# Kernel optimization log

Measured on AMD Instinct MI355X. Metric: run time of the kernel, lower is better.

## Reference

```python
import jax, jax.numpy as jnp
import numpy as np

N = 100000        # nodes
E = 1600000       # edges
G = 128           # graphs in batch
D_FEAT = 240      # continuous node features (input_features - 1)
EMB = 16          # node-type embedding dim
H = 256           # hidden size (both layers)
PH = 128          # pool / classifier hidden
GF = 32           # global feature dim
LN_EPS = 1e-5


def setup_inputs() -> dict:
    key = jax.random.key(0)
    ks = jax.random.split(key, 24)

    node_types = jax.random.randint(ks[0], (N,), 0, 400).astype(jnp.float32)
    feats = jax.random.normal(ks[1], (N, D_FEAT), dtype=jnp.float32)
    x = jnp.concatenate([node_types[:, None], feats], axis=1)  # [N, 241]

    edge_index = jax.random.randint(ks[2], (2, E), 0, N, dtype=jnp.int32)
    batch = jnp.sort(jax.random.randint(ks[3], (N,), 0, G, dtype=jnp.int32))
    global_features = jax.random.normal(ks[4], (G, GF), dtype=jnp.float32)

    s = 0.05
    p = {}
    p['emb_table'] = jax.random.normal(ks[5], (400, EMB), dtype=jnp.float32) * s
    # layer 0 GIN MLP (in=256 -> 256 -> 256) + LayerNorm
    p['l0_w1'] = jax.random.normal(ks[6], (H, H), dtype=jnp.float32) * s
    p['l0_b1'] = jnp.zeros((H,), jnp.float32)
    p['l0_w2'] = jax.random.normal(ks[7], (H, H), dtype=jnp.float32) * s
    p['l0_b2'] = jnp.zeros((H,), jnp.float32)
    p['ln0_g'] = jnp.ones((H,), jnp.float32)
    p['ln0_b'] = jnp.zeros((H,), jnp.float32)
    # layer 1
    p['l1_w1'] = jax.random.normal(ks[8], (H, H), dtype=jnp.float32) * s
    p['l1_b1'] = jnp.zeros((H,), jnp.float32)
    p['l1_w2'] = jax.random.normal(ks[9], (H, H), dtype=jnp.float32) * s
    p['l1_b2'] = jnp.zeros((H,), jnp.float32)
    p['ln1_g'] = jnp.ones((H,), jnp.float32)
    p['ln1_b'] = jnp.zeros((H,), jnp.float32)
    # attentional aggregation gate: 256 -> 128 -> 1
    p['gate_w1'] = jax.random.normal(ks[10], (H, PH), dtype=jnp.float32) * s
    p['gate_b1'] = jnp.zeros((PH,), jnp.float32)
    p['gate_w2'] = jax.random.normal(ks[11], (PH, 1), dtype=jnp.float32) * s
    p['gate_b2'] = jnp.zeros((1,), jnp.float32)
    # classifier: 256+32 -> 128 -> 2
    p['cls_w1'] = jax.random.normal(ks[12], (H + GF, PH), dtype=jnp.float32) * s
    p['cls_b1'] = jnp.zeros((PH,), jnp.float32)
    p['cls_w2'] = jax.random.normal(ks[13], (PH, 2), dtype=jnp.float32) * s
    p['cls_b2'] = jnp.zeros((2,), jnp.float32)

    return dict(x=x, edge_index=edge_index, batch=batch,
                global_features=global_features, **p)


def _layernorm(z, g, b):
    mu = jnp.mean(z, axis=-1, keepdims=True)
    var = jnp.mean(jnp.square(z - mu), axis=-1, keepdims=True)
    return (z - mu) * jax.lax.rsqrt(var + LN_EPS) * g + b


def _gin_block(h, src, dst, w1, b1, w2, b2, ln_g, ln_b):
    # GINConv, eps=0: mlp((1+eps)*x_i + sum_{j->i} x_j)
    agg = jax.ops.segment_sum(h[src], dst, num_segments=h.shape[0])
    z = h + agg
    z = jax.nn.relu(z @ w1 + b1) @ w2 + b2
    z = jax.nn.relu(_layernorm(z, ln_g, ln_b))
    return h + z  # dropout is identity in eval; residual


def reference(x, edge_index, batch, global_features, emb_table,
              l0_w1, l0_b1, l0_w2, l0_b2, ln0_g, ln0_b,
              l1_w1, l1_b1, l1_w2, l1_b2, ln1_g, ln1_b,
              gate_w1, gate_b1, gate_w2, gate_b2,
              cls_w1, cls_b1, cls_w2, cls_b2):
    node_types = x[:, 0].astype(jnp.int32)
    h = jnp.concatenate([x[:, 1:], emb_table[node_types]], axis=1)  # [N, 256]

    src, dst = edge_index[0], edge_index[1]
    h = _gin_block(h, src, dst, l0_w1, l0_b1, l0_w2, l0_b2, ln0_g, ln0_b)
    h = _gin_block(h, src, dst, l1_w1, l1_b1, l1_w2, l1_b2, ln1_g, ln1_b)

    # AttentionalAggregation: segment softmax over gate scores, weighted sum
    gate = jax.nn.relu(h @ gate_w1 + gate_b1) @ gate_w2 + gate_b2  # [N, 1]
    gate = gate[:, 0]
    m = jax.ops.segment_max(gate, batch, num_segments=G)
    a = jnp.exp(gate - m[batch])
    s = jax.ops.segment_sum(a, batch, num_segments=G)
    w = a / s[batch]
    pooled = jax.ops.segment_sum(w[:, None] * h, batch, num_segments=G)  # [G, 256]

    z = jnp.concatenate([pooled, global_features], axis=1)  # [G, 288]
    out = jax.nn.relu(z @ cls_w1 + cls_b1) @ cls_w2 + cls_b2  # [G, 2]
    return out
```

## Files before the change

kernel.cpp:

```cpp
#include <hip/hip_runtime.h>
#include <math.h>

#define N_NODES 100000
#define N_EDGES 1600000
#define NG      128
#define HD      256
#define PHD     128
#define GFD     32
#define XW      241
#define LN_EPS  1e-5f
#define SLOT    64

typedef __attribute__((ext_vector_type(8))) short bf8_t;
typedef __attribute__((ext_vector_type(4))) float f4_t;

static __device__ __forceinline__ float relu_f(float x){ return fmaxf(x, 0.0f); }

static __device__ __forceinline__ unsigned short f2bf_rn(float v) {
    unsigned int u = __float_as_uint(v);
    unsigned int r = (u + 0x7fffu + ((u >> 16) & 1u)) >> 16;
    return (unsigned short)r;
}
static __device__ __forceinline__ float bf2f(unsigned short h) {
    return __uint_as_float((unsigned int)h << 16);
}

__global__ void build_h_kernel(const float* __restrict__ x, const float* __restrict__ emb,
                               float* __restrict__ h, unsigned short* __restrict__ h16)
{
    int node = blockIdx.x;
    int tid  = threadIdx.x;
    const float* xr = x + (size_t)node * XW;
    float v;
    if (tid < 240) {
        v = xr[1 + tid];
    } else {
        int t = (int)xr[0];
        v = emb[t * 16 + (tid - 240)];
    }
    h[(size_t)node * HD + tid] = v;
    h16[(size_t)node * HD + tid] = f2bf_rn(v);
}

__global__ void fill_slots_kernel(const int* __restrict__ src, const int* __restrict__ dst,
                                  int* __restrict__ cnt, int* __restrict__ col, int e)
{
    int i = blockIdx.x * blockDim.x + threadIdx.x;
    if (i < e) {
        int d = dst[i];
        int p = atomicAdd(&cnt[d], 1);
        if (p < SLOT) col[(size_t)d * SLOT + p] = src[i];
    }
}

__global__ __launch_bounds__(256) void aggregate_kernel(
    const float* __restrict__ h, const unsigned short* __restrict__ h16,
    const int* __restrict__ cnt, const int* __restrict__ col,
    float* __restrict__ z, int n)
{
    int node = blockIdx.x * 4 + (threadIdx.x >> 6);
    int lane = threadIdx.x & 63;
    if (node >= n) return;
    const int l4 = lane * 4;
    size_t base = (size_t)node * HD + l4;
    float4 a0 = *(const float4*)&h[base];
    float4 a1 = make_float4(0,0,0,0), a2 = make_float4(0,0,0,0), a3 = make_float4(0,0,0,0);
    int deg = cnt[node]; if (deg > SLOT) deg = SLOT;
    const int* cb = col + (size_t)node * SLOT;
    int e = 0;
    for (; e + 4 <= deg; e += 4) {
        int s0 = cb[e], s1 = cb[e+1], s2 = cb[e+2], s3 = cb[e+3];
        ushort4 u0 = *(const ushort4*)&h16[(size_t)s0 * HD + l4];
        ushort4 u1 = *(const ushort4*)&h16[(size_t)s1 * HD + l4];
        ushort4 u2 = *(const ushort4*)&h16[(size_t)s2 * HD + l4];
        ushort4 u3 = *(const ushort4*)&h16[(size_t)s3 * HD + l4];
        a0.x += bf2f(u0.x); a0.y += bf2f(u0.y); a0.z += bf2f(u0.z); a0.w += bf2f(u0.w);
        a1.x += bf2f(u1.x); a1.y += bf2f(u1.y); a1.z += bf2f(u1.z); a1.w += bf2f(u1.w);
        a2.x += bf2f(u2.x); a2.y += bf2f(u2.y); a2.z += bf2f(u2.z); a2.w += bf2f(u2.w);
        a3.x += bf2f(u3.x); a3.y += bf2f(u3.y); a3.z += bf2f(u3.z); a3.w += bf2f(u3.w);
    }
    for (; e < deg; e++) {
        int s = cb[e];
        ushort4 u = *(const ushort4*)&h16[(size_t)s * HD + l4];
        a0.x += bf2f(u.x); a0.y += bf2f(u.y); a0.z += bf2f(u.z); a0.w += bf2f(u.w);
    }
    a0.x += a1.x + a2.x + a3.x;
    a0.y += a1.y + a2.y + a3.y;
    a0.z += a1.z + a2.z + a3.z;
    a0.w += a1.w + a2.w + a3.w;
    *(float4*)&z[base] = a0;
}

static __device__ __forceinline__ void pack_one(const float* __restrict__ w, short* __restrict__ hi,
                                                int N, int fbase)
{
    int lane = threadIdx.x & 63;
    int f = fbase * 4 + (threadIdx.x >> 6);
    const int KB = 8;
    int nb = f / KB, kb = f % KB;
    int n = nb * 16 + (lane & 15);
    int k0 = kb * 32 + (lane >> 4) * 8;
    size_t o = (size_t)f * 512 + lane * 8;
    #pragma unroll
    for (int j = 0; j < 8; j++) {
        float v = w[(size_t)(k0 + j) * N + n];
        hi[o + j] = (short)f2bf_rn(v);
    }
}

__global__ __launch_bounds__(256) void pack_all_kernel(
    const float* __restrict__ w0, const float* __restrict__ w1,
    const float* __restrict__ w2, const float* __restrict__ w3,
    const float* __restrict__ w4,
    short* o0h, short* o1h, short* o2h, short* o3h, short* o4h)
{
    int b = blockIdx.x;
    if      (b < 32)  pack_one(w0, o0h, HD,  b);
    else if (b < 64)  pack_one(w1, o1h, HD,  b - 32);
    else if (b < 96)  pack_one(w2, o2h, HD,  b - 64);
    else if (b < 128) pack_one(w3, o3h, HD,  b - 96);
    else              pack_one(w4, o4h, PHD, b - 128);
}

static __device__ __forceinline__ void mm32(
    f4_t (&acc)[2][4], const char* buf,
    const short* __restrict__ Bh,
    int wc, int cb, int kg, int lane)
{
    bf8_t bcur[4], bnxt[4];
    #pragma unroll
    for (int ni = 0; ni < 4; ni++)
        bcur[ni] = *(const bf8_t*)&Bh[((size_t)((wc*4+ni)*8))*512 + lane*8];
    for (int kb = 0; kb < 8; kb++) {
        if (kb < 7) {
            #pragma unroll
            for (int ni = 0; ni < 4; ni++)
                bnxt[ni] = *(const bf8_t*)&Bh[((size_t)((wc*4+ni)*8 + kb+1))*512 + lane*8];
        }
        bf8_t ahi[2], alo[2];
        #pragma unroll
        for (int mi = 0; mi < 2; mi++) {
            int row = mi*16 + cb;
            int byte = (row*512 + kb*64 + kg*16) ^ ((row & 7) << 4);
            ahi[mi] = *(const bf8_t*)(buf + byte);
            alo[mi] = *(const bf8_t*)(buf + 16384 + byte);
        }
        #pragma unroll
        for (int mi = 0; mi < 2; mi++)
            #pragma unroll
            for (int ni = 0; ni < 4; ni++)
                acc[mi][ni] = __builtin_amdgcn_mfma_f32_16x16x32_bf16(ahi[mi], bcur[ni], acc[mi][ni], 0, 0, 0);
        #pragma unroll
        for (int mi = 0; mi < 2; mi++)
            #pragma unroll
            for (int ni = 0; ni < 4; ni++)
                acc[mi][ni] = __builtin_amdgcn_mfma_f32_16x16x32_bf16(alo[mi], bcur[ni], acc[mi][ni], 0, 0, 0);
        #pragma unroll
        for (int ni = 0; ni < 4; ni++) bcur[ni] = bnxt[ni];
    }
}

__global__ __launch_bounds__(256, 4) void mlp_mfma_kernel(
    float* __restrict__ h, unsigned short* __restrict__ h16, const float* __restrict__ z,
    const short* __restrict__ w1h, const float* __restrict__ b1,
    const short* __restrict__ w2h, const float* __restrict__ b2,
    const float* __restrict__ lng, const float* __restrict__ lnb)
{
    __shared__ char buf[32768];
    const int tid  = threadIdx.x;
    const int lane = tid & 63;
    const int wv   = tid >> 6;
    const int cb   = lane & 15;
    const int kg   = lane >> 4;
    const long row0 = (long)blockIdx.x * 32;

    for (int rr = 0; rr < 8; rr++) {
        int row = wv * 8 + rr;
        long grow = row0 + row;
        float4 v = make_float4(0.f, 0.f, 0.f, 0.f);
        if (grow < N_NODES) v = *(const float4*)&z[grow * HD + lane * 4];
        ushort4 hi4, lo4;
        unsigned short hb;
        hb = f2bf_rn(v.x); hi4.x = hb; lo4.x = f2bf_rn(v.x - bf2f(hb));
        hb = f2bf_rn(v.y); hi4.y = hb; lo4.y = f2bf_rn(v.y - bf2f(hb));
        hb = f2bf_rn(v.z); hi4.z = hb; lo4.z = f2bf_rn(v.z - bf2f(hb));
        hb = f2bf_rn(v.w); hi4.w = hb; lo4.w = f2bf_rn(v.w - bf2f(hb));
        int byte = (row * 512 + lane * 8) ^ ((row & 7) << 4);
        *(ushort4*)(buf + byte)         = hi4;
        *(ushort4*)(buf + 16384 + byte) = lo4;
    }
    __syncthreads();

    f4_t acc[2][4];
    const f4_t zero4 = {0.f, 0.f, 0.f, 0.f};
    #pragma unroll
    for (int mi = 0; mi < 2; mi++)
        #pragma unroll
        for (int ni = 0; ni < 4; ni++) acc[mi][ni] = zero4;

    mm32(acc, buf, w1h, wv, cb, kg, lane);
    __syncthreads();

    {
        float bias1[4];
        #pragma unroll
        for (int ni = 0; ni < 4; ni++) bias1[ni] = b1[wv * 64 + ni * 16 + cb];
        #pragma unroll
        for (int mi = 0; mi < 2; mi++) {
            #pragma unroll
            for (int ni = 0; ni < 4; ni++) {
                int colx2 = (wv * 64 + ni * 16 + cb) * 2;
                #pragma unroll
                for (int j = 0; j < 4; j++) {
                    float t = relu_f(acc[mi][ni][j] + bias1[ni]);
                    int row = mi * 16 + kg * 4 + j;
                    unsigned short hb = f2bf_rn(t);
                    unsigned short lb = f2bf_rn(t - bf2f(hb));
                    int byte = (row * 512 + colx2) ^ ((row & 7) << 4);
                    *(short*)(buf + byte)         = (short)hb;
                    *(short*)(buf + 16384 + byte) = (short)lb;
                }
            }
        }
    }
    __syncthreads();

    #pragma unroll
    for (int mi = 0; mi < 2; mi++)
        #pragma unroll
        for (int ni = 0; ni < 4; ni++) acc[mi][ni] = zero4;

    mm32(acc, buf, w2h, wv, cb, kg, lane);
    __syncthreads();

    {
        float bias2[4];
        #pragma unroll
        for (int ni = 0; ni < 4; ni++) bias2[ni] = b2[wv * 64 + ni * 16 + cb];
        #pragma unroll
        for (int mi = 0; mi < 2; mi++) {
            #pragma unroll
            for (int ni = 0; ni < 4; ni++) {
                int col = wv * 64 + ni * 16 + cb;
                #pragma unroll
                for (int j = 0; j < 4; j++) {
                    int row = mi * 16 + kg * 4 + j;
                    int byte = (row * 1024 + col * 4) ^ (((row >> 2) & 3) << 6);
                    *(float*)(buf + byte) = acc[mi][ni][j] + bias2[ni];
                }
            }
        }
    }
    __syncthreads();

    {
        const float4 gv = *(const float4*)&lng[lane * 4];
        const float4 bv = *(const float4*)&lnb[lane * 4];
        for (int rr = 0; rr < 8; rr++) {
            int row = wv * 8 + rr;
            long grow = row0 + row;
            if (grow >= N_NODES) break;
            int byte = (row * 1024 + lane * 16) ^ (((row >> 2) & 3) << 6);
            float4 v = *(const float4*)(buf + byte);
            float s = v.x + v.y + v.z + v.w;
            float q = v.x * v.x + v.y * v.y + v.z * v.z + v.w * v.w;
            #pragma unroll
            for (int off = 32; off > 0; off >>= 1) {
                s += __shfl_xor(s, off, 64);
                q += __shfl_xor(q, off, 64);
            }
            float mu = s * (1.0f / 256.0f);
            float var = q * (1.0f / 256.0f) - mu * mu;
            float rstd = rsqrtf(var + LN_EPS);
            size_t gi = (size_t)grow * HD + lane * 4;
            float4 hv = *(float4*)&h[gi];
            hv.x += relu_f((v.x - mu) * rstd * gv.x + bv.x);
            hv.y += relu_f((v.y - mu) * rstd * gv.y + bv.y);
            hv.z += relu_f((v.z - mu) * rstd * gv.z + bv.z);
            hv.w += relu_f((v.w - mu) * rstd * gv.w + bv.w);
            *(float4*)&h[gi] = hv;
            ushort4 m16;
            m16.x = f2bf_rn(hv.x); m16.y = f2bf_rn(hv.y);
            m16.z = f2bf_rn(hv.z); m16.w = f2bf_rn(hv.w);
            *(ushort4*)&h16[gi] = m16;
        }
    }
}

__global__ __launch_bounds__(256, 2) void gate_mfma_kernel(
    const float* __restrict__ h,
    const short* __restrict__ g1h, const float* __restrict__ gb1,
    const float* __restrict__ gw2, const float* __restrict__ gb2,
    float* __restrict__ gate)
{
    __shared__ char buf[65536];
    const int tid  = threadIdx.x;
    const int lane = tid & 63;
    const int wv   = tid >> 6;
    const int cb   = lane & 15;
    const int kg   = lane >> 4;
    const long row0 = (long)blockIdx.x * 64;

    for (int rr = 0; rr < 16; rr++) {
        int row = wv * 16 + rr;
        long grow = row0 + row;
        float4 v = make_float4(0.f, 0.f, 0.f, 0.f);
        if (grow < N_NODES) v = *(const float4*)&h[grow * HD + lane * 4];
        ushort4 hi4, lo4;
        unsigned short hb;
        hb = f2bf_rn(v.x); hi4.x = hb; lo4.x = f2bf_rn(v.x - bf2f(hb));
        hb = f2bf_rn(v.y); hi4.y = hb; lo4.y = f2bf_rn(v.y - bf2f(hb));
        hb = f2bf_rn(v.z); hi4.z = hb; lo4.z = f2bf_rn(v.z - bf2f(hb));
        hb = f2bf_rn(v.w); hi4.w = hb; lo4.w = f2bf_rn(v.w - bf2f(hb));
        int byte = (row * 512 + lane * 8) ^ ((row & 7) << 4);
        *(ushort4*)(buf + byte)         = hi4;
        *(ushort4*)(buf + 32768 + byte) = lo4;
    }
    __syncthreads();

    f4_t acc[4][2];
    const f4_t zero4 = {0.f, 0.f, 0.f, 0.f};
    #pragma unroll
    for (int mi = 0; mi < 4; mi++) { acc[mi][0] = zero4; acc[mi][1] = zero4; }

    #pragma unroll
    for (int pass = 0; pass < 2; pass++) {
        const char* Abase = (pass == 1) ? (buf + 32768) : buf;
        for (int kb = 0; kb < 8; kb++) {
            bf8_t a[4], b[2];
            #pragma unroll
            for (int mi = 0; mi < 4; mi++) {
                int row = mi * 16 + cb;
                int byte = (row * 512 + kb * 64 + kg * 16) ^ ((row & 7) << 4);
                a[mi] = *(const bf8_t*)(Abase + byte);
            }
            #pragma unroll
            for (int ni = 0; ni < 2; ni++) {
                int nb = wv * 2 + ni;
                b[ni] = *(const bf8_t*)&g1h[(size_t)(nb * 8 + kb) * 512 + lane * 8];
            }
            #pragma unroll
            for (int mi = 0; mi < 4; mi++)
                #pragma unroll
                for (int ni = 0; ni < 2; ni++)
                    acc[mi][ni] = __builtin_amdgcn_mfma_f32_16x16x32_bf16(a[mi], b[ni], acc[mi][ni], 0, 0, 0);
        }
    }
    __syncthreads();

    {
        float* G1 = (float*)buf;
        float bias1[2];
        bias1[0] = gb1[wv * 32 + cb];
        bias1[1] = gb1[wv * 32 + 16 + cb];
        #pragma unroll
        for (int mi = 0; mi < 4; mi++) {
            #pragma unroll
            for (int ni = 0; ni < 2; ni++) {
                int colv = wv * 32 + ni * 16 + cb;
                #pragma unroll
                for (int j = 0; j < 4; j++) {
                    int row = mi * 16 + kg * 4 + j;
                    G1[row * PHD + colv] = relu_f(acc[mi][ni][j] + bias1[ni]);
                }
            }
        }
    }
    __syncthreads();

    {
        const float* G1 = (const float*)buf;
        float2 wv2 = *(const float2*)&gw2[lane * 2];
        float b2v = gb2[0];
        for (int rr = 0; rr < 16; rr++) {
            int row = wv * 16 + rr;
            long grow = row0 + row;
            if (grow >= N_NODES) break;
            float2 t2 = *(const float2*)&G1[row * PHD + lane * 2];
            float p = t2.x * wv2.x + t2.y * wv2.y;
            #pragma unroll
            for (int off = 32; off > 0; off >>= 1) p += __shfl_xor(p, off, 64);
            if (lane == 0) gate[grow] = p + b2v;
        }
    }
}

__global__ void goff_kernel(const int* __restrict__ batch, int* __restrict__ goff, int n)
{
    int t = threadIdx.x;
    if (t > NG) return;
    int lo = 0, hi = n;
    while (lo < hi) {
        int mid = (lo + hi) >> 1;
        if (batch[mid] < t) lo = mid + 1; else hi = mid;
    }
    goff[t] = lo;
}

__global__ __launch_bounds__(256) void pool_kernel(
    const float* __restrict__ h, const float* __restrict__ gate,
    const int* __restrict__ goff, float* __restrict__ pooled)
{
    __shared__ float red[256];
    __shared__ float m_sh, s_sh;
    int g = blockIdx.x >> 2, q = blockIdx.x & 3;
    int tid = threadIdx.x;
    int beg = goff[g], end = goff[g + 1];
    if (beg >= end) return;

    float lm = -3.4e38f;
    for (int i = beg + tid; i < end; i += 256) lm = fmaxf(lm, gate[i]);
    red[tid] = lm; __syncthreads();
    for (int off = 128; off > 0; off >>= 1) {
        if (tid < off) red[tid] = fmaxf(red[tid], red[tid + off]);
        __syncthreads();
    }
    if (tid == 0) m_sh = red[0];
    __syncthreads();
    float m = m_sh;

    float ls = 0.0f;
    for (int i = beg + tid; i < end; i += 256) ls += expf(gate[i] - m);
    __syncthreads();
    red[tid] = ls; __syncthreads();
    for (int off = 128; off > 0; off >>= 1) {
        if (tid < off) red[tid] += red[tid + off];
        __syncthreads();
    }
    if (tid == 0) s_sh = red[0];
    __syncthreads();
    float inv_s = 1.0f / s_sh;

    float acc = 0.0f;
    for (int i = beg + q; i < end; i += 4) {
        float a = expf(gate[i] - m);
        acc += a * h[(size_t)i * HD + tid];
    }
    atomicAdd(&pooled[(size_t)g * HD + tid], acc * inv_s);
}

__global__ __launch_bounds__(128) void cls_kernel(
    const float* __restrict__ pooled, const float* __restrict__ gf,
    const float* __restrict__ w1, const float* __restrict__ b1,
    const float* __restrict__ w2, const float* __restrict__ b2,
    float* __restrict__ out)
{
    __shared__ float r0[128], r1[128];
    int g = blockIdx.x, c = threadIdx.x;
    float acc = b1[c];
    const float* pr = pooled + (size_t)g * HD;
    for (int k = 0; k < HD; k++) acc += pr[k] * w1[k * PHD + c];
    const float* gr = gf + g * GFD;
    for (int k = 0; k < GFD; k++) acc += gr[k] * w1[(HD + k) * PHD + c];
    float t = relu_f(acc);
    r0[c] = t * w2[c * 2 + 0];
    r1[c] = t * w2[c * 2 + 1];
    __syncthreads();
    for (int off = 64; off > 0; off >>= 1) {
        if (c < off) { r0[c] += r0[c + off]; r1[c] += r1[c + off]; }
        __syncthreads();
    }
    if (c == 0) {
        out[g * 2 + 0] = r0[0] + b2[0];
        out[g * 2 + 1] = r1[0] + b2[1];
    }
}

extern "C" void kernel_launch(void* const* d_in, const int* in_sizes, int n_in,
                              void* d_out, int out_size, void* d_ws, size_t ws_size,
                              hipStream_t stream)
{
    const float* x    = (const float*)d_in[0];
    const int*   ei   = (const int*)d_in[1];
    const int*   bat  = (const int*)d_in[2];
    const float* gf   = (const float*)d_in[3];
    const float* emb  = (const float*)d_in[4];
    const float* l0w1 = (const float*)d_in[5];
    const float* l0b1 = (const float*)d_in[6];
    const float* l0w2 = (const float*)d_in[7];
    const float* l0b2 = (const float*)d_in[8];
    const float* ln0g = (const float*)d_in[9];
    const float* ln0b = (const float*)d_in[10];
    const float* l1w1 = (const float*)d_in[11];
    const float* l1b1 = (const float*)d_in[12];
    const float* l1w2 = (const float*)d_in[13];
    const float* l1b2 = (const float*)d_in[14];
    const float* ln1g = (const float*)d_in[15];
    const float* ln1b = (const float*)d_in[16];
    const float* gw1  = (const float*)d_in[17];
    const float* gb1  = (const float*)d_in[18];
    const float* gw2  = (const float*)d_in[19];
    const float* gb2  = (const float*)d_in[20];
    const float* cw1  = (const float*)d_in[21];
    const float* cb1  = (const float*)d_in[22];
    const float* cw2  = (const float*)d_in[23];
    const float* cb2  = (const float*)d_in[24];

    char* ws = (char*)d_ws;
    size_t off = 0;
    auto alloc = [&](size_t bytes) {
        void* p = ws + off;
        off += (bytes + 255) & ~(size_t)255;
        return p;
    };
    float* h      = (float*)alloc((size_t)N_NODES * HD * 4);
    unsigned short* h16 = (unsigned short*)alloc((size_t)N_NODES * HD * 2);
    float* z      = (float*)alloc((size_t)N_NODES * HD * 4);
    float* gate   = (float*)alloc((size_t)N_NODES * 4);
    int*   cnt    = (int*)alloc((size_t)N_NODES * 4);
    int*   col    = (int*)alloc((size_t)N_NODES * SLOT * 4);
    int*   goff   = (int*)alloc((NG + 1) * 4);
    float* pooled = (float*)alloc((size_t)NG * HD * 4);
    short* p_l0w1h = (short*)alloc((size_t)HD * HD * 2);
    short* p_l0w2h = (short*)alloc((size_t)HD * HD * 2);
    short* p_l1w1h = (short*)alloc((size_t)HD * HD * 2);
    short* p_l1w2h = (short*)alloc((size_t)HD * HD * 2);
    short* p_gw1h  = (short*)alloc((size_t)HD * PHD * 2);

    const int* src = ei;
    const int* dst = ei + N_EDGES;

    build_h_kernel<<<N_NODES, 256, 0, stream>>>(x, emb, h, h16);

    hipMemsetAsync(cnt, 0, (size_t)N_NODES * 4, stream);
    fill_slots_kernel<<<(N_EDGES + 255) / 256, 256, 0, stream>>>(src, dst, cnt, col, N_EDGES);

    pack_all_kernel<<<144, 256, 0, stream>>>(l0w1, l0w2, l1w1, l1w2, gw1,
                                             p_l0w1h, p_l0w2h, p_l1w1h, p_l1w2h, p_gw1h);

    const int mlp_grid = (N_NODES + 31) / 32;

    aggregate_kernel<<<N_NODES / 4, 256, 0, stream>>>(h, h16, cnt, col, z, N_NODES);
    mlp_mfma_kernel<<<mlp_grid, 256, 0, stream>>>(h, h16, z, p_l0w1h, l0b1,
                                                  p_l0w2h, l0b2, ln0g, ln0b);
    aggregate_kernel<<<N_NODES / 4, 256, 0, stream>>>(h, h16, cnt, col, z, N_NODES);
    mlp_mfma_kernel<<<mlp_grid, 256, 0, stream>>>(h, h16, z, p_l1w1h, l1b1,
                                                  p_l1w2h, l1b2, ln1g, ln1b);

    gate_mfma_kernel<<<(N_NODES + 63) / 64, 256, 0, stream>>>(h, p_gw1h, gb1, gw2, gb2, gate);
    goff_kernel<<<1, 256, 0, stream>>>(bat, goff, N_NODES);
    hipMemsetAsync(pooled, 0, (size_t)NG * HD * 4, stream);
    pool_kernel<<<NG * 4, 256, 0, stream>>>(h, gate, goff, pooled);
    cls_kernel<<<NG, 128, 0, stream>>>(pooled, gf, cw1, cb1, cw2, cb2, (float*)d_out);
}
```

Measured before the change: 806.1 us.

## Fuse neighbor aggregation into GIN MLP kernel with ping-pong bf16 buffers

Folds the gather-and-sum aggregation into the MLP kernel's staging loop, so each block aggregates its own 32 rows directly into shared memory instead of writing and rereading a full fp32 z buffer. Double-buffered bf16 copies of h keep a layer's gathers from reading rows it has already updated. This removes a global round trip of the N x 256 fp32 intermediate and two launches. The risk is that the MFMA kernel, limited to 4 blocks per CU, now carries latency-bound random gathers and may lose the occupancy the standalone aggregate kernel had for hiding them. Bounds checks are dropped because N is divisible by 32.

Result: faster. 769.7 us (-4.5%).

```diff
diff --git a/kernel.cpp b/kernel.cpp
--- a/kernel.cpp
+++ b/kernel.cpp
@@ -51,44 +51,6 @@
         int p = atomicAdd(&cnt[d], 1);
         if (p < SLOT) col[(size_t)d * SLOT + p] = src[i];
     }
-}
-
-__global__ __launch_bounds__(256) void aggregate_kernel(
-    const float* __restrict__ h, const unsigned short* __restrict__ h16,
-    const int* __restrict__ cnt, const int* __restrict__ col,
-    float* __restrict__ z, int n)
-{
-    int node = blockIdx.x * 4 + (threadIdx.x >> 6);
-    int lane = threadIdx.x & 63;
-    if (node >= n) return;
-    const int l4 = lane * 4;
-    size_t base = (size_t)node * HD + l4;
-    float4 a0 = *(const float4*)&h[base];
-    float4 a1 = make_float4(0,0,0,0), a2 = make_float4(0,0,0,0), a3 = make_float4(0,0,0,0);
-    int deg = cnt[node]; if (deg > SLOT) deg = SLOT;
-    const int* cb = col + (size_t)node * SLOT;
-    int e = 0;
-    for (; e + 4 <= deg; e += 4) {
-        int s0 = cb[e], s1 = cb[e+1], s2 = cb[e+2], s3 = cb[e+3];
-        ushort4 u0 = *(const ushort4*)&h16[(size_t)s0 * HD + l4];
-        ushort4 u1 = *(const ushort4*)&h16[(size_t)s1 * HD + l4];
-        ushort4 u2 = *(const ushort4*)&h16[(size_t)s2 * HD + l4];
-        ushort4 u3 = *(const ushort4*)&h16[(size_t)s3 * HD + l4];
-        a0.x += bf2f(u0.x); a0.y += bf2f(u0.y); a0.z += bf2f(u0.z); a0.w += bf2f(u0.w);
-        a1.x += bf2f(u1.x); a1.y += bf2f(u1.y); a1.z += bf2f(u1.z); a1.w += bf2f(u1.w);
-        a2.x += bf2f(u2.x); a2.y += bf2f(u2.y); a2.z += bf2f(u2.z); a2.w += bf2f(u2.w);
-        a3.x += bf2f(u3.x); a3.y += bf2f(u3.y); a3.z += bf2f(u3.z); a3.w += bf2f(u3.w);
-    }
-    for (; e < deg; e++) {
-        int s = cb[e];
-        ushort4 u = *(const ushort4*)&h16[(size_t)s * HD + l4];
-        a0.x += bf2f(u.x); a0.y += bf2f(u.y); a0.z += bf2f(u.z); a0.w += bf2f(u.w);
-    }
-    a0.x += a1.x + a2.x + a3.x;
-    a0.y += a1.y + a2.y + a3.y;
-    a0.z += a1.z + a2.z + a3.z;
-    a0.w += a1.w + a2.w + a3.w;
-    *(float4*)&z[base] = a0;
 }
 
 static __device__ __forceinline__ void pack_one(const float* __restrict__ w, short* __restrict__ hi,
@@ -160,8 +122,10 @@
     }
 }
 
-__global__ __launch_bounds__(256, 4) void mlp_mfma_kernel(
-    float* __restrict__ h, unsigned short* __restrict__ h16, const float* __restrict__ z,
+__global__ __launch_bounds__(256, 4) void gin_layer_kernel(
+    float* __restrict__ h, const unsigned short* __restrict__ h16i,
+    unsigned short* __restrict__ h16o,
+    const int* __restrict__ cnt, const int* __restrict__ col,
     const short* __restrict__ w1h, const float* __restrict__ b1,
     const short* __restrict__ w2h, const float* __restrict__ b2,
     const float* __restrict__ lng, const float* __restrict__ lnb)
@@ -172,19 +136,43 @@
     const int wv   = tid >> 6;
     const int cb   = lane & 15;
     const int kg   = lane >> 4;
+    const int l4   = lane * 4;
     const long row0 = (long)blockIdx.x * 32;
 
     for (int rr = 0; rr < 8; rr++) {
         int row = wv * 8 + rr;
         long grow = row0 + row;
-        float4 v = make_float4(0.f, 0.f, 0.f, 0.f);
-        if (grow < N_NODES) v = *(const float4*)&z[grow * HD + lane * 4];
+        float4 a0 = *(const float4*)&h[grow * HD + l4];
+        float4 a1 = make_float4(0,0,0,0), a2 = make_float4(0,0,0,0), a3 = make_float4(0,0,0,0);
+        int deg = cnt[grow]; if (deg > SLOT) deg = SLOT;
+        const int* cb4 = col + (size_t)grow * SLOT;
+        int e = 0;
+        for (; e + 4 <= deg; e += 4) {
+            int s0 = cb4[e], s1 = cb4[e+1], s2 = cb4[e+2], s3 = cb4[e+3];
+            ushort4 u0 = *(const ushort4*)&h16i[(size_t)s0 * HD + l4];
+            ushort4 u1 = *(const ushort4*)&h16i[(size_t)s1 * HD + l4];
+            ushort4 u2 = *(const ushort4*)&h16i[(size_t)s2 * HD + l4];
+            ushort4 u3 = *(const ushort4*)&h16i[(size_t)s3 * HD + l4];
+            a0.x += bf2f(u0.x); a0.y += bf2f(u0.y); a0.z += bf2f(u0.z); a0.w += bf2f(u0.w);
+            a1.x += bf2f(u1.x); a1.y += bf2f(u1.y); a1.z += bf2f(u1.z); a1.w += bf2f(u1.w);
+            a2.x += bf2f(u2.x); a2.y += bf2f(u2.y); a2.z += bf2f(u2.z); a2.w += bf2f(u2.w);
+            a3.x += bf2f(u3.x); a3.y += bf2f(u3.y); a3.z += bf2f(u3.z); a3.w += bf2f(u3.w);
+        }
+        for (; e < deg; e++) {
+            int s = cb4[e];
+            ushort4 u = *(const ushort4*)&h16i[(size_t)s * HD + l4];
+            a0.x += bf2f(u.x); a0.y += bf2f(u.y); a0.z += bf2f(u.z); a0.w += bf2f(u.w);
+        }
+        a0.x += a1.x + a2.x + a3.x;
+        a0.y += a1.y + a2.y + a3.y;
+        a0.z += a1.z + a2.z + a3.z;
+        a0.w += a1.w + a2.w + a3.w;
         ushort4 hi4, lo4;
         unsigned short hb;
-        hb = f2bf_rn(v.x); hi4.x = hb; lo4.x = f2bf_rn(v.x - bf2f(hb));
-        hb = f2bf_rn(v.y); hi4.y = hb; lo4.y = f2bf_rn(v.y - bf2f(hb));
-        hb = f2bf_rn(v.z); hi4.z = hb; lo4.z = f2bf_rn(v.z - bf2f(hb));
-        hb = f2bf_rn(v.w); hi4.w = hb; lo4.w = f2bf_rn(v.w - bf2f(hb));
+        hb = f2bf_rn(a0.x); hi4.x = hb; lo4.x = f2bf_rn(a0.x - bf2f(hb));
+        hb = f2bf_rn(a0.y); hi4.y = hb; lo4.y = f2bf_rn(a0.y - bf2f(hb));
+        hb = f2bf_rn(a0.z); hi4.z = hb; lo4.z = f2bf_rn(a0.z - bf2f(hb));
+        hb = f2bf_rn(a0.w); hi4.w = hb; lo4.w = f2bf_rn(a0.w - bf2f(hb));
         int byte = (row * 512 + lane * 8) ^ ((row & 7) << 4);
         *(ushort4*)(buf + byte)         = hi4;
         *(ushort4*)(buf + 16384 + byte) = lo4;
@@ -241,11 +229,11 @@
         for (int mi = 0; mi < 2; mi++) {
             #pragma unroll
             for (int ni = 0; ni < 4; ni++) {
-                int col = wv * 64 + ni * 16 + cb;
+                int col2 = wv * 64 + ni * 16 + cb;
                 #pragma unroll
                 for (int j = 0; j < 4; j++) {
                     int row = mi * 16 + kg * 4 + j;
-                    int byte = (row * 1024 + col * 4) ^ (((row >> 2) & 3) << 6);
+                    int byte = (row * 1024 + col2 * 4) ^ (((row >> 2) & 3) << 6);
                     *(float*)(buf + byte) = acc[mi][ni][j] + bias2[ni];
                 }
             }
@@ -254,12 +242,11 @@
     __syncthreads();
 
     {
-        const float4 gv = *(const float4*)&lng[lane * 4];
-        const float4 bv = *(const float4*)&lnb[lane * 4];
+        const float4 gv = *(const float4*)&lng[l4];
+        const float4 bv = *(const float4*)&lnb[l4];
         for (int rr = 0; rr < 8; rr++) {
             int row = wv * 8 + rr;
             long grow = row0 + row;
-            if (grow >= N_NODES) break;
             int byte = (row * 1024 + lane * 16) ^ (((row >> 2) & 3) << 6);
             float4 v = *(const float4*)(buf + byte);
             float s = v.x + v.y + v.z + v.w;
@@ -272,7 +259,7 @@
             float mu = s * (1.0f / 256.0f);
             float var = q * (1.0f / 256.0f) - mu * mu;
             float rstd = rsqrtf(var + LN_EPS);
-            size_t gi = (size_t)grow * HD + lane * 4;
+            size_t gi = (size_t)grow * HD + l4;
             float4 hv = *(float4*)&h[gi];
             hv.x += relu_f((v.x - mu) * rstd * gv.x + bv.x);
             hv.y += relu_f((v.y - mu) * rstd * gv.y + bv.y);
@@ -282,7 +269,7 @@
             ushort4 m16;
             m16.x = f2bf_rn(hv.x); m16.y = f2bf_rn(hv.y);
             m16.z = f2bf_rn(hv.z); m16.w = f2bf_rn(hv.w);
-            *(ushort4*)&h16[gi] = m16;
+            *(ushort4*)&h16o[gi] = m16;
         }
     }
 }
@@ -504,8 +491,8 @@
         return p;
     };
     float* h      = (float*)alloc((size_t)N_NODES * HD * 4);
-    unsigned short* h16 = (unsigned short*)alloc((size_t)N_NODES * HD * 2);
-    float* z      = (float*)alloc((size_t)N_NODES * HD * 4);
+    unsigned short* h16a = (unsigned short*)alloc((size_t)N_NODES * HD * 2);
+    unsigned short* h16b = (unsigned short*)alloc((size_t)N_NODES * HD * 2);
     float* gate   = (float*)alloc((size_t)N_NODES * 4);
     int*   cnt    = (int*)alloc((size_t)N_NODES * 4);
     int*   col    = (int*)alloc((size_t)N_NODES * SLOT * 4);
@@ -520,7 +507,7 @@
     const int* src = ei;
     const int* dst = ei + N_EDGES;
 
-    build_h_kernel<<<N_NODES, 256, 0, stream>>>(x, emb, h, h16);
+    build_h_kernel<<<N_NODES, 256, 0, stream>>>(x, emb, h, h16a);
 
     hipMemsetAsync(cnt, 0, (size_t)N_NODES * 4, stream);
     fill_slots_kernel<<<(N_EDGES + 255) / 256, 256, 0, stream>>>(src, dst, cnt, col, N_EDGES);
@@ -528,14 +515,12 @@
     pack_all_kernel<<<144, 256, 0, stream>>>(l0w1, l0w2, l1w1, l1w2, gw1,
                                              p_l0w1h, p_l0w2h, p_l1w1h, p_l1w2h, p_gw1h);
 
-    const int mlp_grid = (N_NODES + 31) / 32;
-
-    aggregate_kernel<<<N_NODES / 4, 256, 0, stream>>>(h, h16, cnt, col, z, N_NODES);
-    mlp_mfma_kernel<<<mlp_grid, 256, 0, stream>>>(h, h16, z, p_l0w1h, l0b1,
-                                                  p_l0w2h, l0b2, ln0g, ln0b);
-    aggregate_kernel<<<N_NODES / 4, 256, 0, stream>>>(h, h16, cnt, col, z, N_NODES);
-    mlp_mfma_kernel<<<mlp_grid, 256, 0, stream>>>(h, h16, z, p_l1w1h, l1b1,
-                                                  p_l1w2h, l1b2, ln1g, ln1b);
+    const int layer_grid = N_NODES / 32;
+
+    gin_layer_kernel<<<layer_grid, 256, 0, stream>>>(h, h16a, h16b, cnt, col,
+                                                     p_l0w1h, l0b1, p_l0w2h, l0b2, ln0g, ln0b);
+    gin_layer_kernel<<<layer_grid, 256, 0, stream>>>(h, h16b, h16a, cnt, col,
+                                                     p_l1w1h, l1b1, p_l1w2h, l1b2, ln1g, ln1b);
 
     gate_mfma_kernel<<<(N_NODES + 63) / 64, 256, 0, stream>>>(h, p_gw1h, gb1, gw2, gb2, gate);
     goff_kernel<<<1, 256, 0, stream>>>(bat, goff, N_NODES);
```
